# Optimization experiments

Measured on AMD Instinct MI355X. Metric: run time of the kernel, lower is better.

Reference implementation:

```python
import jax, jax.numpy as jnp
import numpy as np


def setup_inputs() -> dict:
    key = jax.random.key(0)
    ks = jax.random.split(key, 7)
    B, T, E, D = 4, 4096, 1024, 64
    s = 1.0 / np.sqrt(E)
    return {
        "x": jax.random.normal(ks[0], (B, T, E), dtype=jnp.float32),
        "Wq": jax.random.normal(ks[1], (E, D), dtype=jnp.float32) * s,
        "bq": jnp.zeros((D,), dtype=jnp.float32),
        "Wk": jax.random.normal(ks[2], (E, D), dtype=jnp.float32) * s,
        "bk": jnp.zeros((D,), dtype=jnp.float32),
        "Wv": jax.random.normal(ks[3], (E, D), dtype=jnp.float32) * s,
        "bv": jnp.zeros((D,), dtype=jnp.float32),
    }


def reference(x, Wq, bq, Wk, bk, Wv, bv):
    # Linear projections (torch Linear with W stored as [in, out])
    q = x @ Wq + bq  # [B, T, D]
    k = x @ Wk + bk  # [B, T, D]
    v = x @ Wv + bv  # [B, T, D]
    d_k = q.shape[-1]
    scale = 1.0 / jnp.sqrt(jnp.asarray(d_k, dtype=q.dtype))
    scores = jnp.einsum("btd,bsd->bts", q, k) * scale  # [B, T, T]
    att = jax.nn.softmax(scores, axis=-1)
    # dropout p=0.0 -> identity (eval-mode reference)
    out = jnp.einsum("bts,bsd->btd", att, v)  # [B, T, D]
    return out
```

## Files before the change

kernel.cpp:

```cpp
#include <hip/hip_runtime.h>

typedef __attribute__((ext_vector_type(4))) float f32x4;
typedef __attribute__((ext_vector_type(16))) float f32x16;
typedef __attribute__((ext_vector_type(8))) short s16x8;
typedef __attribute__((ext_vector_type(4))) short s16x4;
typedef __attribute__((ext_vector_type(4))) unsigned u32x4;

#define BATCH 4
#define SEQ 4096
#define EMB 1024
#define HD 64
#define QSCALE (0.125f * 1.44269504088896f)

static __device__ __forceinline__ unsigned short f2bf(float f) {
  union { float f; unsigned int u; } a;
  a.f = f;
  unsigned int u = a.u;
  u += 0x7FFFu + ((u >> 16) & 1u);
  return (unsigned short)(u >> 16);
}

static __device__ __forceinline__ float fexp2(float x) {
  float r;
  asm("v_exp_f32 %0, %1\n\ts_nop 0" : "=v"(r) : "v"(x));
  return r;
}
static __device__ __forceinline__ void swap32f(float& a, float& b) {
  asm("s_nop 0\n\tv_permlane32_swap_b32 %0, %1\n\ts_nop 0" : "+v"(a), "+v"(b));
}
static __device__ __forceinline__ void swap32u(unsigned& a, unsigned& b) {
  asm("s_nop 0\n\tv_permlane32_swap_b32 %0, %1\n\ts_nop 0" : "+v"(a), "+v"(b));
}
static __device__ __forceinline__ unsigned cvtpk(float lo, float hi) {
  unsigned r;
  asm("v_cvt_pk_bf16_f32 %0, %1, %2" : "=v"(r) : "v"(lo), "v"(hi));
  return r;
}

#define GLL16(g, l)                                                        \
  __builtin_amdgcn_global_load_lds(                                        \
      (const __attribute__((address_space(1))) unsigned int*)(g),          \
      (__attribute__((address_space(3))) unsigned int*)(l), 16, 0, 0)

__global__ __launch_bounds__(256) void k_wt(const float* __restrict__ Wq,
                                            const float* __restrict__ Wk,
                                            const float* __restrict__ Wv,
                                            unsigned short* __restrict__ wt) {
  __shared__ float lds[64][65];
  int tid = threadIdx.x;
  int which = blockIdx.x >> 4;
  int kt = blockIdx.x & 15;
  const float* W = (which == 0) ? Wq : ((which == 1) ? Wk : Wv);
#pragma unroll
  for (int i = 0; i < 4; ++i) {
    int idx = i * 256 + tid;
    int row = idx >> 4, c4 = idx & 15;
    float4 v = *(const float4*)(W + (size_t)(kt * 64 + row) * 64 + c4 * 4);
    lds[row][c4 * 4 + 0] = v.x;
    lds[row][c4 * 4 + 1] = v.y;
    lds[row][c4 * 4 + 2] = v.z;
    lds[row][c4 * 4 + 3] = v.w;
  }
  __syncthreads();
#pragma unroll
  for (int i = 0; i < 2; ++i) {
    int c = i * 256 + tid;
    int cfl = c >> 7, kk = (c >> 6) & 1, l = c & 63;
    int lg = l >> 4, lc = l & 15;
    s16x8 v;
#pragma unroll
    for (int j = 0; j < 8; ++j) v[j] = (short)f2bf(lds[kk * 32 + lg * 8 + j][cfl * 16 + lc]);
    size_t off = ((((size_t)kt * 12 + (which * 4 + cfl)) * 2 + kk) * 64 + l) * 8;
    *(s16x8*)(wt + off) = v;
  }
}

__global__ __launch_bounds__(256, 2) void k_proj(const float* __restrict__ x,
                                                 const unsigned short* __restrict__ wt,
                                                 const float* __restrict__ bq,
                                                 const float* __restrict__ bk,
                                                 const float* __restrict__ bv,
                                                 unsigned short* __restrict__ qws,
                                                 unsigned short* __restrict__ kws,
                                                 unsigned short* __restrict__ vws) {
  __shared__ char xb[4][8192];
  int tid = threadIdx.x;
  int w = tid >> 6, ln = tid & 63;
  int lg = ln >> 4, lc = ln & 15;
  int m0 = blockIdx.x * 32;

  f32x4 acc[2][3];
#pragma unroll
  for (int s = 0; s < 2; ++s)
#pragma unroll
    for (int c = 0; c < 3; ++c) acc[s][c] = (f32x4){0.f, 0.f, 0.f, 0.f};

  s16x8 bA[3][2], bB[3][2];

  int srow = w * 8 + (ln >> 4);
  int schunk0 = ln & 15;
#define GLLI(kt_, bi_)                                                        \
  _Pragma("unroll") for (int p = 0; p < 2; ++p) {                             \
    int r = srow + p * 4;                                                     \
    const char* src = (const char*)x + (size_t)(m0 + r) * 4096 + (kt_)*256 +  \
                      ((schunk0 ^ (r & 7)) << 4);                             \
    GLL16(src, &xb[bi_][w * 2048 + p * 1024]);                                \
  }
#define BLD(dst_, kt_)                                                        \
  _Pragma("unroll") for (int c = 0; c < 3; ++c)                               \
      _Pragma("unroll") for (int kk = 0; kk < 2; ++kk)                        \
          dst_[c][kk] = *(const s16x8*)(wt + ((size_t)((kt_)*12 + w * 3 + c) * 2 + kk) * 512 + ln * 8);

#define ITER(T_, bcur_, bnext_, NW_)                                          \
  {                                                                           \
    if ((T_) + 1 < 16) BLD(bnext_, (T_) + 1);                                 \
    if ((T_) + 3 < 16) GLLI((T_) + 3, ((T_) + 3) & 3);                        \
    asm volatile("s_waitcnt vmcnt(" #NW_ ")" ::: "memory");                   \
    __builtin_amdgcn_s_barrier();                                             \
    __builtin_amdgcn_sched_barrier(0);                                        \
    s16x8 a[2][2];                                                            \
    _Pragma("unroll") for (int s = 0; s < 2; ++s)                             \
        _Pragma("unroll") for (int kk = 0; kk < 2; ++kk) {                    \
      int g0 = kk * 8 + lg * 2;                                               \
      f32x4 c0 = *(const f32x4*)(&xb[(T_) & 3][(s * 16 + lc) * 256 + ((g0 ^ (lc & 7)) << 4)]); \
      f32x4 c1 = *(const f32x4*)(&xb[(T_) & 3][(s * 16 + lc) * 256 + (((g0 + 1) ^ (lc & 7)) << 4)]); \
      union { u32x4 u; s16x8 v; } cv;                                         \
      cv.u = (u32x4){cvtpk(c0[0], c0[1]), cvtpk(c0[2], c0[3]),                \
                     cvtpk(c1[0], c1[1]), cvtpk(c1[2], c1[3])};               \
      a[s][kk] = cv.v;                                                        \
    }                                                                         \
    __builtin_amdgcn_s_setprio(1);                                            \
    _Pragma("unroll") for (int s = 0; s < 2; ++s)                             \
        _Pragma("unroll") for (int c = 0; c < 3; ++c)                         \
            _Pragma("unroll") for (int kk = 0; kk < 2; ++kk)                  \
                acc[s][c] = __builtin_amdgcn_mfma_f32_16x16x32_bf16(          \
                    a[s][kk], bcur_[c][kk], acc[s][c], 0, 0, 0);              \
    __builtin_amdgcn_s_setprio(0);                                            \
    __builtin_amdgcn_s_barrier();                                             \
  }

  GLLI(0, 0);
  GLLI(1, 1);
  GLLI(2, 2);
  BLD(bA, 0);
  ITER(0, bA, bB, 18)
  ITER(1, bB, bA, 24)
  ITER(2, bA, bB, 30)
  ITER(3, bB, bA, 24)
  ITER(4, bA, bB, 24)
  ITER(5, bB, bA, 24)
  ITER(6, bA, bB, 24)
  ITER(7, bB, bA, 24)
  ITER(8, bA, bB, 24)
  ITER(9, bB, bA, 24)
  ITER(10, bA, bB, 24)
  ITER(11, bB, bA, 24)
  ITER(12, bA, bB, 24)
  ITER(13, bB, bA, 22)
  ITER(14, bA, bB, 20)
  ITER(15, bB, bA, 12)
#undef GLLI
#undef BLD
#undef ITER

  unsigned short* ep = (unsigned short*)&xb[0][0];
#pragma unroll
  for (int c = 0; c < 3; ++c) {
    int cf = w * 3 + c;
    int which = cf >> 2;
    int ncol = (cf & 3) * 16 + lc;
    float bias = (which == 0) ? bq[ncol] : ((which == 1) ? bk[ncol] : bv[ncol]);
    if (which < 2) {
#pragma unroll
      for (int s = 0; s < 2; ++s)
#pragma unroll
        for (int r = 0; r < 4; ++r) {
          int trow = s * 16 + lg * 4 + r;
          float val = acc[s][c][r] + bias;
          if (which == 0) val *= QSCALE;
          int o = (ncol >> 4) * 512 + ((ncol >> 3) & 1) * 256 + trow * 8 + (ncol & 7);
          ep[which * 2048 + o] = f2bf(val);
        }
    } else {
#pragma unroll
      for (int s = 0; s < 2; ++s) {
        s16x4 pk;
#pragma unroll
        for (int r = 0; r < 4; ++r) pk[r] = (short)f2bf(acc[s][c][r] + bias);
        int o = s * 1024 + (ncol >> 5) * 512 + (lg >> 1) * 256 + (ncol & 31) * 8 + (lg & 1) * 4;
        *(s16x4*)(ep + 2 * 2048 + o) = pk;
      }
    }
  }
  __syncthreads();
  {
    int b = m0 >> 12, tt = m0 & 4095;
    unsigned short* qdst = qws + (size_t)b * SEQ * 64 + (tt >> 5) * 2048;
    unsigned short* kdst = kws + (size_t)b * SEQ * 64 + (tt >> 5) * 2048;
    unsigned short* vdst = vws + (size_t)b * SEQ * 64 + (tt >> 4) * 1024;
#pragma unroll
    for (int k = 0; k < 3; ++k) {
      int u = k * 256 + tid;
      s16x8 val = *(const s16x8*)(ep + u * 8);
      int which = u >> 8;
      int o = (u & 255) * 8;
      unsigned short* dst = (which == 0) ? qdst : ((which == 1) ? kdst : vdst);
      *(s16x8*)(dst + o) = val;
    }
  }
}

template <int NS>
__global__ __launch_bounds__(256, 2) void k_attn(const unsigned short* __restrict__ qf_g,
                                                 const unsigned short* __restrict__ kf_g,
                                                 const unsigned short* __restrict__ vf_g,
                                                 float* __restrict__ part,
                                                 float2* __restrict__ ml) {
  int tid = threadIdx.x;
  int w = tid >> 6, ln = tid & 63;
  int F = blockIdx.x;
  int chunk = 8 * NS;
  int idx = (F & 7) * chunk + (F >> 3);
  int split = idx >> 6;
  int rem = idx & 63;
  int b = rem >> 4, q16 = rem & 15;
  const int TPS = 64 / NS;
  int t0 = split * TPS;
  int tlast = t0 + TPS - 1;

  const unsigned short* qb = qf_g + (size_t)b * SEQ * 64;
  const unsigned short* kb = kf_g + (size_t)b * SEQ * 64;
  const unsigned short* vb = vf_g + (size_t)b * SEQ * 64;

  int qrow = q16 * 256 + w * 64;

  s16x8 qf[2][4];
#pragma unroll
  for (int sub = 0; sub < 2; ++sub)
#pragma unroll
    for (int db = 0; db < 4; ++db)
      qf[sub][db] = *(const s16x8*)(qb + (size_t)(((q16 * 8 + w * 2 + sub) * 4 + db) * 512 + ln * 8));

  f32x16 o_[2][2];
#pragma unroll
  for (int sub = 0; sub < 2; ++sub)
#pragma unroll
    for (int dt = 0; dt < 2; ++dt)
#pragma unroll
      for (int i = 0; i < 16; ++i) o_[sub][dt][i] = 0.f;
  float m_[2] = {-1e30f, -1e30f}, l_[2] = {0.f, 0.f};

  s16x8 kfc[2][4];
#pragma unroll
  for (int kt = 0; kt < 2; ++kt)
#pragma unroll
    for (int db = 0; db < 4; ++db)
      kfc[kt][db] = *(const s16x8*)(kb + (size_t)(((t0 * 2 + kt) * 4 + db) * 512 + ln * 8));

#pragma unroll 1
  for (int t = t0; t <= tlast; ++t) {
    f32x16 s0[2];
    __builtin_amdgcn_s_setprio(1);
#pragma unroll
    for (int kt = 0; kt < 2; ++kt) {
      f32x16 a = {0.f, 0.f, 0.f, 0.f, 0.f, 0.f, 0.f, 0.f,
                  0.f, 0.f, 0.f, 0.f, 0.f, 0.f, 0.f, 0.f};
#pragma unroll
      for (int db = 0; db < 4; ++db)
        a = __builtin_amdgcn_mfma_f32_32x32x16_bf16(kfc[kt][db], qf[0][db], a, 0, 0, 0);
      s0[kt] = a;
    }
    __builtin_amdgcn_s_setprio(0);

    s16x8 vf[4][2];
#pragma unroll
    for (int k4 = 0; k4 < 4; ++k4)
#pragma unroll
      for (int dt = 0; dt < 2; ++dt)
        vf[k4][dt] = *(const s16x8*)(vb + (size_t)(((t * 4 + k4) * 2 + dt) * 512 + ln * 8));

    s16x8 pf[2][4];
#define SOFTMAX_PACK(S_, SUBIDX)                                               \
    {                                                                          \
      float mx[16];                                                            \
      _Pragma("unroll") for (int i = 0; i < 16; ++i)                           \
          mx[i] = fmaxf(S_[0][i], S_[1][i]);                                   \
      _Pragma("unroll") for (int i = 0; i < 8; ++i) mx[i] = fmaxf(mx[i], mx[i + 8]); \
      _Pragma("unroll") for (int i = 0; i < 4; ++i) mx[i] = fmaxf(mx[i], mx[i + 4]); \
      float tm = fmaxf(fmaxf(mx[0], mx[1]), fmaxf(mx[2], mx[3]));              \
      float ta = tm, tb = tm;                                                  \
      swap32f(ta, tb);                                                         \
      tm = fmaxf(ta, tb);                                                      \
      if (!__all(tm <= m_[SUBIDX] + 8.0f)) {                                   \
        float mn = fmaxf(m_[SUBIDX], tm);                                      \
        float al = fexp2(m_[SUBIDX] - mn);                                     \
        _Pragma("unroll") for (int dt = 0; dt < 2; ++dt)                       \
            _Pragma("unroll") for (int i = 0; i < 16; ++i) o_[SUBIDX][dt][i] *= al; \
        l_[SUBIDX] *= al;                                                      \
        m_[SUBIDX] = mn;                                                       \
      }                                                                        \
      float mm = m_[SUBIDX];                                                   \
      _Pragma("unroll") for (int kt = 0; kt < 2; ++kt)                         \
          _Pragma("unroll") for (int i = 0; i < 16; ++i)                       \
              S_[kt][i] = fexp2(S_[kt][i] - mm);                               \
      float sm[16];                                                            \
      _Pragma("unroll") for (int i = 0; i < 16; ++i) sm[i] = S_[0][i] + S_[1][i]; \
      _Pragma("unroll") for (int i = 0; i < 8; ++i) sm[i] += sm[i + 8];        \
      _Pragma("unroll") for (int i = 0; i < 4; ++i) sm[i] += sm[i + 4];        \
      float ts = (sm[0] + sm[1]) + (sm[2] + sm[3]);                            \
      float sa = ts, sb = ts;                                                  \
      swap32f(sa, sb);                                                         \
      l_[SUBIDX] += sa + sb;                                                   \
      _Pragma("unroll") for (int k4 = 0; k4 < 4; ++k4) {                       \
        int kt = k4 >> 1, mr = 2 * (k4 & 1);                                   \
        unsigned a0 = cvtpk(S_[kt][mr * 4 + 0], S_[kt][mr * 4 + 1]);           \
        unsigned a1 = cvtpk(S_[kt][mr * 4 + 2], S_[kt][mr * 4 + 3]);           \
        unsigned b0 = cvtpk(S_[kt][mr * 4 + 4], S_[kt][mr * 4 + 5]);           \
        unsigned b1 = cvtpk(S_[kt][mr * 4 + 6], S_[kt][mr * 4 + 7]);           \
        swap32u(a0, b0);                                                       \
        swap32u(a1, b1);                                                       \
        union { u32x4 u; s16x8 v16; } cvt;                                     \
        cvt.u = (u32x4){a0, a1, b0, b1};                                       \
        pf[SUBIDX][k4] = cvt.v16;                                              \
      }                                                                        \
    }

    SOFTMAX_PACK(s0, 0)

    f32x16 s1[2];
    __builtin_amdgcn_s_setprio(1);
#pragma unroll
    for (int kt = 0; kt < 2; ++kt) {
      f32x16 a = {0.f, 0.f, 0.f, 0.f, 0.f, 0.f, 0.f, 0.f,
                  0.f, 0.f, 0.f, 0.f, 0.f, 0.f, 0.f, 0.f};
#pragma unroll
      for (int db = 0; db < 4; ++db)
        a = __builtin_amdgcn_mfma_f32_32x32x16_bf16(kfc[kt][db], qf[1][db], a, 0, 0, 0);
      s1[kt] = a;
    }
    __builtin_amdgcn_s_setprio(0);

    {
      int tn = t < tlast ? t + 1 : tlast;
#pragma unroll
      for (int kt = 0; kt < 2; ++kt)
#pragma unroll
        for (int db = 0; db < 4; ++db)
          kfc[kt][db] = *(const s16x8*)(kb + (size_t)(((tn * 2 + kt) * 4 + db) * 512 + ln * 8));
    }

    SOFTMAX_PACK(s1, 1)
#undef SOFTMAX_PACK

    __builtin_amdgcn_s_setprio(1);
#pragma unroll
    for (int sub = 0; sub < 2; ++sub)
#pragma unroll
      for (int dt = 0; dt < 2; ++dt)
#pragma unroll
        for (int k4 = 0; k4 < 4; ++k4)
          o_[sub][dt] = __builtin_amdgcn_mfma_f32_32x32x16_bf16(vf[k4][dt], pf[sub][k4],
                                                                o_[sub][dt], 0, 0, 0);
    __builtin_amdgcn_s_setprio(0);
  }

  float* pb = part + (size_t)(split * 4 + b) * 64 * SEQ;
  int hi = ln >> 5, lq = ln & 31;
#pragma unroll
  for (int sub = 0; sub < 2; ++sub) {
    int tq = qrow + sub * 32 + lq;
#pragma unroll
    for (int dt = 0; dt < 2; ++dt)
#pragma unroll
      for (int re = 0; re < 16; ++re) {
        int d = dt * 32 + (re & 3) + 8 * (re >> 2) + 4 * hi;
        pb[(size_t)d * SEQ + tq] = o_[sub][dt][re];
      }
  }
  if (ln < 32) {
#pragma unroll
    for (int sub = 0; sub < 2; ++sub)
      ml[(size_t)(split * 4 + b) * SEQ + qrow + sub * 32 + ln] = make_float2(m_[sub], l_[sub]);
  }
}

template <int NS>
__global__ __launch_bounds__(256) void k_red(const float* __restrict__ part,
                                             const float2* __restrict__ ml,
                                             float* __restrict__ out) {
  __shared__ float lds[64][65];
  int tid = threadIdx.x;
  int w = tid >> 6, ln = tid & 63;
  int t0 = blockIdx.x * 64;
  int b = t0 >> 12, tt = t0 & 4095;
  int t = tt + ln;

  float2 mls[NS];
#pragma unroll
  for (int s = 0; s < NS; ++s) mls[s] = ml[(size_t)(s * 4 + b) * SEQ + t];
  float M = mls[0].x;
#pragma unroll
  for (int s = 1; s < NS; ++s) M = fmaxf(M, mls[s].x);
  float Lden = 0.f;
#pragma unroll
  for (int s = 0; s < NS; ++s) Lden += mls[s].y * fexp2(mls[s].x - M);
  float inv = 1.0f / Lden;
  float sc[NS];
#pragma unroll
  for (int s = 0; s < NS; ++s) sc[s] = fexp2(mls[s].x - M) * inv;

  float acc[16];
#pragma unroll
  for (int i = 0; i < 16; ++i) acc[i] = 0.f;
#pragma unroll
  for (int s = 0; s < NS; ++s) {
    const float* pb = part + ((size_t)(s * 4 + b) * 64 + w * 16) * SEQ + t;
#pragma unroll
    for (int i = 0; i < 16; ++i) acc[i] += sc[s] * pb[(size_t)i * SEQ];
  }
#pragma unroll
  for (int i = 0; i < 16; ++i) lds[w * 16 + i][ln] = acc[i];
  __syncthreads();
#pragma unroll
  for (int r = 0; r < 16; ++r)
    out[(size_t)(t0 + w * 16 + r) * 64 + ln] = lds[ln][w * 16 + r];
}

extern "C" void kernel_launch(void* const* d_in, const int* in_sizes, int n_in,
                              void* d_out, int out_size, void* d_ws, size_t ws_size,
                              hipStream_t stream) {
  const float* x = (const float*)d_in[0];
  const float* Wq = (const float*)d_in[1];
  const float* bq = (const float*)d_in[2];
  const float* Wk = (const float*)d_in[3];
  const float* bk = (const float*)d_in[4];
  const float* Wv = (const float*)d_in[5];
  const float* bv = (const float*)d_in[6];
  float* out = (float*)d_out;

  char* ws = (char*)d_ws;
  unsigned short* wt = (unsigned short*)(ws);
  unsigned short* qws = (unsigned short*)(ws + 0x80000);
  unsigned short* kws = (unsigned short*)(ws + 0x280000);
  unsigned short* vws = (unsigned short*)(ws + 0x480000);
  const size_t base = 0x680000;
  const size_t perSplit = (size_t)16384 * 64 * 4 + (size_t)16384 * 8;

  k_wt<<<48, 256, 0, stream>>>(Wq, Wk, Wv, wt);
  k_proj<<<512, 256, 0, stream>>>(x, wt, bq, bk, bv, qws, kws, vws);

#define RUN_NS(NSV)                                                           \
  {                                                                           \
    float* partp = (float*)(ws + base);                                       \
    float2* mlp = (float2*)(ws + base + (size_t)NSV * 16384 * 64 * 4);        \
    k_attn<NSV><<<64 * NSV, 256, 0, stream>>>(qws, kws, vws, partp, mlp);     \
    k_red<NSV><<<256, 256, 0, stream>>>(partp, mlp, out);                     \
  }

  if (ws_size >= base + 8 * perSplit) {
    RUN_NS(8)
  } else if (ws_size >= base + 4 * perSplit) {
    RUN_NS(4)
  } else if (ws_size >= base + 2 * perSplit) {
    RUN_NS(2)
  } else {
    RUN_NS(1)
  }
#undef RUN_NS
}
```

Measured before the change: 62.53 us.

## Stage K/V tiles through double-buffered LDS with direct global-to-LDS loads

Before this change, each of the four waves loaded K and V fragments straight from global memory on its own, so every block read the same K/V tile four times. Now the block cooperatively copies each 16KB K+V tile into a double-buffered shared-memory array using direct global-to-LDS loads. The next tile is prefetched while the current one is consumed, with vmcnt waits and barriers for synchronization. This cuts redundant global and L2 traffic, but adds two block barriers per iteration and 32KB of LDS per block, which could limit occupancy at two blocks per CU.

Result: no change. 62.08 us (-0.7%).

```diff
diff --git a/kernel.cpp b/kernel.cpp
--- a/kernel.cpp
+++ b/kernel.cpp
@@ -216,6 +216,7 @@
                                                  const unsigned short* __restrict__ vf_g,
                                                  float* __restrict__ part,
                                                  float2* __restrict__ ml) {
+  __shared__ char kv[2][16384];
   int tid = threadIdx.x;
   int w = tid >> 6, ln = tid & 63;
   int F = blockIdx.x;
@@ -229,8 +230,8 @@
   int tlast = t0 + TPS - 1;
 
   const unsigned short* qb = qf_g + (size_t)b * SEQ * 64;
-  const unsigned short* kb = kf_g + (size_t)b * SEQ * 64;
-  const unsigned short* vb = vf_g + (size_t)b * SEQ * 64;
+  const char* kbytes = (const char*)(kf_g + (size_t)b * SEQ * 64);
+  const char* vbytes = (const char*)(vf_g + (size_t)b * SEQ * 64);
 
   int qrow = q16 * 256 + w * 64;
 
@@ -250,15 +251,35 @@
       for (int i = 0; i < 16; ++i) o_[sub][dt][i] = 0.f;
   float m_[2] = {-1e30f, -1e30f}, l_[2] = {0.f, 0.f};
 
-  s16x8 kfc[2][4];
-#pragma unroll
-  for (int kt = 0; kt < 2; ++kt)
-#pragma unroll
-    for (int db = 0; db < 4; ++db)
-      kfc[kt][db] = *(const s16x8*)(kb + (size_t)(((t0 * 2 + kt) * 4 + db) * 512 + ln * 8));
-
+#define STAGE(t_, bi_)                                                        \
+  _Pragma("unroll") for (int i = 0; i < 4; ++i) {                             \
+    int cc = w * 4 + i;                                                       \
+    const char* src = (cc < 8 ? kbytes + (size_t)(t_)*8192 + cc * 1024        \
+                              : vbytes + (size_t)(t_)*8192 + (cc - 8) * 1024) \
+                      + ln * 16;                                              \
+    GLL16(src, &kv[bi_][cc * 1024]);                                          \
+  }
+
+  STAGE(t0, 0)
 #pragma unroll 1
   for (int t = t0; t <= tlast; ++t) {
+    int bi = (t - t0) & 1;
+    if (t < tlast) {
+      STAGE(t + 1, bi ^ 1)
+      asm volatile("s_waitcnt vmcnt(4)" ::: "memory");
+    } else {
+      asm volatile("s_waitcnt vmcnt(0)" ::: "memory");
+    }
+    __builtin_amdgcn_s_barrier();
+    __builtin_amdgcn_sched_barrier(0);
+
+    s16x8 kfc[2][4];
+#pragma unroll
+    for (int kt = 0; kt < 2; ++kt)
+#pragma unroll
+      for (int db = 0; db < 4; ++db)
+        kfc[kt][db] = *(const s16x8*)(&kv[bi][(kt * 4 + db) * 1024 + ln * 16]);
+
     f32x16 s0[2];
     __builtin_amdgcn_s_setprio(1);
 #pragma unroll
@@ -277,7 +298,7 @@
     for (int k4 = 0; k4 < 4; ++k4)
 #pragma unroll
       for (int dt = 0; dt < 2; ++dt)
-        vf[k4][dt] = *(const s16x8*)(vb + (size_t)(((t * 4 + k4) * 2 + dt) * 512 + ln * 8));
+        vf[k4][dt] = *(const s16x8*)(&kv[bi][8192 + (k4 * 2 + dt) * 1024 + ln * 16]);
 
     s16x8 pf[2][4];
 #define SOFTMAX_PACK(S_, SUBIDX)                                               \
@@ -340,15 +361,6 @@
     }
     __builtin_amdgcn_s_setprio(0);
 
-    {
-      int tn = t < tlast ? t + 1 : tlast;
-#pragma unroll
-      for (int kt = 0; kt < 2; ++kt)
-#pragma unroll
-        for (int db = 0; db < 4; ++db)
-          kfc[kt][db] = *(const s16x8*)(kb + (size_t)(((tn * 2 + kt) * 4 + db) * 512 + ln * 8));
-    }
-
     SOFTMAX_PACK(s1, 1)
 #undef SOFTMAX_PACK
 
@@ -362,7 +374,9 @@
           o_[sub][dt] = __builtin_amdgcn_mfma_f32_32x32x16_bf16(vf[k4][dt], pf[sub][k4],
                                                                 o_[sub][dt], 0, 0, 0);
     __builtin_amdgcn_s_setprio(0);
-  }
+    __builtin_amdgcn_s_barrier();
+  }
+#undef STAGE
 
   float* pb = part + (size_t)(split * 4 + b) * 64 * SEQ;
   int hi = ln >> 5, lq = ln & 31;
```
